# Kernel optimization log

Hardware: AMD Instinct MI355X
Metric: run time of the kernel (lower is better)

## Reference

```python
import jax, jax.numpy as jnp
import numpy as np

N_HEAD = 32
HEAD_DIM = 128
D = N_HEAD * HEAD_DIM  # 4096
B = 8
NUM_PAGES = 32
PAGE = 128


def setup_inputs() -> dict:
    key = jax.random.key(0)
    ks = jax.random.split(key, 7)
    s = 0.02
    return {
        "x": jax.random.normal(ks[0], (B, 1, D), jnp.float32),
        "k_cache": jax.random.normal(ks[1], (NUM_PAGES, B, N_HEAD, PAGE, HEAD_DIM), jnp.float32),
        "v_cache": jax.random.normal(ks[2], (NUM_PAGES, B, N_HEAD, PAGE, HEAD_DIM), jnp.float32),
        "w_attn": jax.random.normal(ks[3], (D, 3 * D), jnp.float32) * s,
        "b_attn": jax.random.normal(ks[4], (3 * D,), jnp.float32) * s,
        "w_proj": jax.random.normal(ks[5], (D, D), jnp.float32) * s,
        "b_proj": jax.random.normal(ks[6], (D,), jnp.float32) * s,
    }


def _online_attention(q, k_cache, v_cache, k_cur, v_cur):
    # q, k_cur, v_cur: [B, H, 1, hd]; caches: [P, B, H, page, hd]
    scale = 1.0 / np.sqrt(HEAD_DIM)

    def page_step(carry, kv):
        denom, y = carry  # denom: [B,H,1,1], y: [B,H,1,hd]
        k_i, v_i = kv
        S = jnp.einsum("bhqd,bhkd->bhqk", q, k_i) * scale
        P = jnp.exp(S)  # no running-max, exactly as source
        d = P.sum(axis=-1, keepdims=True)
        y = (jnp.einsum("bhqk,bhkd->bhqd", P, v_i) + denom * y) / (denom + d)
        return (denom + d, y), None

    denom0 = jnp.zeros((q.shape[0], N_HEAD, 1, 1), q.dtype)
    y0 = jnp.zeros_like(q)
    (denom, y), _ = jax.lax.scan(page_step, (denom0, y0), (k_cache, v_cache))
    # final step with current-token k, v
    S_n = jnp.einsum("bhqd,bhkd->bhqk", q, k_cur) * scale
    P_n = jnp.exp(S_n)
    d_n = P_n.sum(axis=-1, keepdims=True)
    y = (jnp.einsum("bhqk,bhkd->bhqd", P_n, v_cur) + denom * y) / (denom + d_n)
    return y


def reference(x, k_cache, v_cache, w_attn, b_attn, w_proj, b_proj):
    Bq, T, _ = x.shape  # T == 1 (decode)
    qkv = x @ w_attn + b_attn  # [B, 1, 3D]
    q, k, v = jnp.split(qkv, 3, axis=-1)
    def heads(t):
        return t.reshape(Bq, T, N_HEAD, HEAD_DIM).transpose(0, 2, 1, 3)  # [B,H,1,hd]
    q, k, v = heads(q), heads(k), heads(v)
    y = _online_attention(q, k_cache, v_cache, k, v)  # [B,H,1,hd]
    y = y.transpose(0, 2, 1, 3).reshape(Bq, 1, D)
    return y @ w_proj + b_proj
```

## Files before the change

### kernel.cpp

```cpp
#include <hip/hip_runtime.h>
#include <math.h>

#define DMODEL 4096
#define THREED 12288
#define NHEAD 32
#define HDIM 128
#define NB 8
#define NPAGES 32
#define PAGEK 128

#if __has_builtin(__builtin_amdgcn_exp2f)
#define FAST_EXP2(x) __builtin_amdgcn_exp2f(x)
#else
#define FAST_EXP2(x) exp2f(x)
#endif

#define SCALE_LOG2E (0.08838834764831845f * 1.44269504088896340736f)

__global__ __launch_bounds__(256) void gemm_skinny_partial(
    const float* __restrict__ X, const float* __restrict__ W,
    float* __restrict__ part, int K, int N, int kchunk) {
  const int col = (blockIdx.x * 256 + threadIdx.x) * 2;
  const int k0 = blockIdx.y * kchunk;

  float2 acc[8];
  #pragma unroll
  for (int b = 0; b < 8; ++b) acc[b] = make_float2(0.f, 0.f);

  const float* wp = W + (size_t)k0 * N + col;
  const float* xp = X + k0;

  #pragma unroll 8
  for (int k = 0; k < kchunk; ++k) {
    const float2 w = *(const float2*)(wp + (size_t)k * N);
    #pragma unroll
    for (int b = 0; b < 8; ++b) {
      const float xv = xp[b * K + k];
      acc[b].x += xv * w.x;
      acc[b].y += xv * w.y;
    }
  }
  #pragma unroll
  for (int b = 0; b < 8; ++b)
    *(float2*)(part + ((size_t)blockIdx.y * 8 + b) * N + col) = acc[b];
}

__global__ __launch_bounds__(256) void gemm_skinny_reduce(
    const float* __restrict__ part, const float* __restrict__ bias,
    float* __restrict__ out, int N, int ksplit) {
  int idx = blockIdx.x * 256 + threadIdx.x;
  int n4 = N >> 2;
  int b = idx / n4, col = (idx - b * n4) * 4;
  float4 acc = *(const float4*)(bias + col);
  for (int s = 0; s < ksplit; ++s) {
    const float4 p = *(const float4*)(part + ((size_t)s * 8 + b) * N + col);
    acc.x += p.x;
    acc.y += p.y;
    acc.z += p.z;
    acc.w += p.w;
  }
  *(float4*)(out + (size_t)b * N + col) = acc;
}

__global__ __launch_bounds__(256) void attn_partial(
    const float* __restrict__ qkv,
    const float* __restrict__ k_cache,
    const float* __restrict__ v_cache,
    float* __restrict__ part_y,
    float* __restrict__ part_den) {
  const int page = blockIdx.x;
  const int h = blockIdx.y;
  const int b = blockIdx.z;
  const int tid = threadIdx.x;
  const int wave = tid >> 6;
  const int lane = tid & 63;
  const int half = lane >> 5;
  const int l31 = lane & 31;

  const float4 qf =
      *(const float4*)(qkv + (size_t)b * THREED + h * HDIM + 4 * l31);

  const size_t base = ((((size_t)page * NB + b) * NHEAD + h) * PAGEK) * HDIM;
  const float* kp = k_cache + base;
  const float* vp = v_cache + base;

  float4 yacc = {0.f, 0.f, 0.f, 0.f};
  float den = 0.f;

  #pragma unroll 8
  for (int i = 0; i < 16; ++i) {
    const int key = wave * 32 + i * 2 + half;
    const float4 kf = *(const float4*)(kp + key * HDIM + 4 * l31);
    const float4 vf = *(const float4*)(vp + key * HDIM + 4 * l31);
    float s = qf.x * kf.x + qf.y * kf.y + qf.z * kf.z + qf.w * kf.w;
    s += __shfl_xor(s, 1, 64);
    s += __shfl_xor(s, 2, 64);
    s += __shfl_xor(s, 4, 64);
    s += __shfl_xor(s, 8, 64);
    s += __shfl_xor(s, 16, 64);
    const float w = FAST_EXP2(s * SCALE_LOG2E);
    den += w;
    yacc.x += w * vf.x;
    yacc.y += w * vf.y;
    yacc.z += w * vf.z;
    yacc.w += w * vf.w;
  }

  __shared__ float y_lds[8][HDIM];
  __shared__ float d_lds[8];
  const int row = wave * 2 + half;
  *(float4*)&y_lds[row][4 * l31] = yacc;
  if (l31 == 0) d_lds[row] = den;
  __syncthreads();

  if (tid < HDIM) {
    float y = 0.f;
    #pragma unroll
    for (int r = 0; r < 8; ++r) y += y_lds[r][tid];
    const int bhp = (b * NHEAD + h) * NPAGES + page;
    part_y[(size_t)bhp * HDIM + tid] = y;
    if (tid == 0) {
      float dd = 0.f;
      #pragma unroll
      for (int r = 0; r < 8; ++r) dd += d_lds[r];
      part_den[bhp] = dd;
    }
  }
}

__global__ __launch_bounds__(128) void attn_reduce(
    const float* __restrict__ qkv,
    const float* __restrict__ part_y, const float* __restrict__ part_den,
    float* __restrict__ yattn) {
  const int h = blockIdx.x;
  const int b = blockIdx.y;
  const int d = threadIdx.x;
  const int bh = b * NHEAD + h;

  float y = 0.f;
  #pragma unroll 4
  for (int p = 0; p < NPAGES; ++p)
    y += part_y[((size_t)bh * NPAGES + p) * HDIM + d];
  float den = 0.f;
  #pragma unroll 4
  for (int p = 0; p < NPAGES; ++p) den += part_den[bh * NPAGES + p];

  const float q = qkv[(size_t)b * THREED + h * HDIM + d];
  const float kc = qkv[(size_t)b * THREED + DMODEL + h * HDIM + d];
  const float vc = qkv[(size_t)b * THREED + 2 * DMODEL + h * HDIM + d];

  __shared__ float red[HDIM];
  red[d] = q * kc;
  __syncthreads();
  for (int s = 64; s > 0; s >>= 1) {
    if (d < s) red[d] += red[d + s];
    __syncthreads();
  }
  const float wn = FAST_EXP2(red[0] * SCALE_LOG2E);
  y = (y + wn * vc) / (den + wn);
  yattn[(size_t)b * DMODEL + h * HDIM + d] = y;
}

extern "C" void kernel_launch(void* const* d_in, const int* in_sizes, int n_in,
                              void* d_out, int out_size, void* d_ws,
                              size_t ws_size, hipStream_t stream) {
  const float* x = (const float*)d_in[0];
  const float* k_cache = (const float*)d_in[1];
  const float* v_cache = (const float*)d_in[2];
  const float* w_attn = (const float*)d_in[3];
  const float* b_attn = (const float*)d_in[4];
  const float* w_proj = (const float*)d_in[5];
  const float* b_proj = (const float*)d_in[6];
  float* out = (float*)d_out;
  float* ws = (float*)d_ws;

  float* qkv = ws;
  float* g1p = qkv + 98304;
  float* apy = g1p + 32 * 8 * THREED;
  float* apd = apy + 8192 * HDIM;
  float* yat = apd + 8192;
  float* g2p = yat + NB * DMODEL;

  gemm_skinny_partial<<<dim3(THREED / 512, 32), 256, 0, stream>>>(
      x, w_attn, g1p, DMODEL, THREED, 128);
  gemm_skinny_reduce<<<dim3(NB * THREED / 1024), 256, 0, stream>>>(
      g1p, b_attn, qkv, THREED, 32);

  attn_partial<<<dim3(NPAGES, NHEAD, NB), 256, 0, stream>>>(
      qkv, k_cache, v_cache, apy, apd);
  attn_reduce<<<dim3(NHEAD, NB), 128, 0, stream>>>(qkv, apy, apd, yat);

  gemm_skinny_partial<<<dim3(DMODEL / 512, 64), 256, 0, stream>>>(
      yat, w_proj, g2p, DMODEL, DMODEL, 64);
  gemm_skinny_reduce<<<dim3(NB * DMODEL / 1024), 256, 0, stream>>>(
      g2p, b_proj, out, DMODEL, 64);
}
```

Before: 275.6 us.

## Fuse QKV reduce and page-split attention into one per-head kernel

Replaces the page-split attention kernel, its reduction kernel and the QKV split-K reduce with one kernel per (head, batch). Each block first sums the split-K partials plus bias for its q/k/v slice, then loops over all pages itself. This drops two launches and the partial-result round trips through memory. In exchange, the attention grid shrinks from thousands of blocks to 256, which risks too little memory-level parallelism to stream the KV cache at full bandwidth.

```diff
diff --git a/kernel.cpp b/kernel.cpp
--- a/kernel.cpp
+++ b/kernel.cpp
@@ -62,103 +62,95 @@
   *(float4*)(out + (size_t)b * N + col) = acc;
 }
 
-__global__ __launch_bounds__(256) void attn_partial(
-    const float* __restrict__ qkv,
+__global__ __launch_bounds__(512) void attn_mono(
+    const float* __restrict__ g1p,
+    const float* __restrict__ b_attn,
     const float* __restrict__ k_cache,
     const float* __restrict__ v_cache,
-    float* __restrict__ part_y,
-    float* __restrict__ part_den) {
-  const int page = blockIdx.x;
-  const int h = blockIdx.y;
-  const int b = blockIdx.z;
+    float* __restrict__ yat) {
+  const int h = blockIdx.x;
+  const int b = blockIdx.y;
   const int tid = threadIdx.x;
-  const int wave = tid >> 6;
+
+  __shared__ float q_lds[HDIM], kc_lds[HDIM], vc_lds[HDIM];
+  __shared__ float y16[16][HDIM];
+  __shared__ float den16[16];
+  __shared__ float wn_lds;
+
+  if (tid < 384) {
+    const int which = tid >> 7;
+    const int d = tid & 127;
+    const int col = which * DMODEL + h * HDIM + d;
+    float val = b_attn[col];
+    #pragma unroll 8
+    for (int s = 0; s < 32; ++s)
+      val += g1p[((size_t)s * 8 + b) * THREED + col];
+    if (which == 0) q_lds[d] = val;
+    else if (which == 1) kc_lds[d] = val;
+    else vc_lds[d] = val;
+  }
+  __syncthreads();
+
+  if (tid < 64) {
+    float s0 = q_lds[tid] * kc_lds[tid] + q_lds[tid + 64] * kc_lds[tid + 64];
+    s0 += __shfl_xor(s0, 1, 64);
+    s0 += __shfl_xor(s0, 2, 64);
+    s0 += __shfl_xor(s0, 4, 64);
+    s0 += __shfl_xor(s0, 8, 64);
+    s0 += __shfl_xor(s0, 16, 64);
+    s0 += __shfl_xor(s0, 32, 64);
+    if (tid == 0) wn_lds = FAST_EXP2(s0 * SCALE_LOG2E);
+  }
+
+  const int wv = tid >> 6;
   const int lane = tid & 63;
   const int half = lane >> 5;
   const int l31 = lane & 31;
-
-  const float4 qf =
-      *(const float4*)(qkv + (size_t)b * THREED + h * HDIM + 4 * l31);
-
-  const size_t base = ((((size_t)page * NB + b) * NHEAD + h) * PAGEK) * HDIM;
-  const float* kp = k_cache + base;
-  const float* vp = v_cache + base;
+  const float4 qf = *(const float4*)&q_lds[4 * l31];
 
   float4 yacc = {0.f, 0.f, 0.f, 0.f};
   float den = 0.f;
 
-  #pragma unroll 8
-  for (int i = 0; i < 16; ++i) {
-    const int key = wave * 32 + i * 2 + half;
-    const float4 kf = *(const float4*)(kp + key * HDIM + 4 * l31);
-    const float4 vf = *(const float4*)(vp + key * HDIM + 4 * l31);
-    float s = qf.x * kf.x + qf.y * kf.y + qf.z * kf.z + qf.w * kf.w;
-    s += __shfl_xor(s, 1, 64);
-    s += __shfl_xor(s, 2, 64);
-    s += __shfl_xor(s, 4, 64);
-    s += __shfl_xor(s, 8, 64);
-    s += __shfl_xor(s, 16, 64);
-    const float w = FAST_EXP2(s * SCALE_LOG2E);
-    den += w;
-    yacc.x += w * vf.x;
-    yacc.y += w * vf.y;
-    yacc.z += w * vf.z;
-    yacc.w += w * vf.w;
+  for (int p = 0; p < NPAGES; ++p) {
+    const size_t base = ((((size_t)p * NB + b) * NHEAD + h) * PAGEK) * HDIM;
+    const float* kp = k_cache + base;
+    const float* vp = v_cache + base;
+    #pragma unroll 8
+    for (int i = 0; i < 8; ++i) {
+      const int key = wv * 16 + i * 2 + half;
+      const float4 kf = *(const float4*)(kp + key * HDIM + 4 * l31);
+      const float4 vf = *(const float4*)(vp + key * HDIM + 4 * l31);
+      float s = qf.x * kf.x + qf.y * kf.y + qf.z * kf.z + qf.w * kf.w;
+      s += __shfl_xor(s, 1, 64);
+      s += __shfl_xor(s, 2, 64);
+      s += __shfl_xor(s, 4, 64);
+      s += __shfl_xor(s, 8, 64);
+      s += __shfl_xor(s, 16, 64);
+      const float w = FAST_EXP2(s * SCALE_LOG2E);
+      den += w;
+      yacc.x += w * vf.x;
+      yacc.y += w * vf.y;
+      yacc.z += w * vf.z;
+      yacc.w += w * vf.w;
+    }
   }
 
-  __shared__ float y_lds[8][HDIM];
-  __shared__ float d_lds[8];
-  const int row = wave * 2 + half;
-  *(float4*)&y_lds[row][4 * l31] = yacc;
-  if (l31 == 0) d_lds[row] = den;
+  const int row = wv * 2 + half;
+  *(float4*)&y16[row][4 * l31] = yacc;
+  if (l31 == 0) den16[row] = den;
   __syncthreads();
 
   if (tid < HDIM) {
     float y = 0.f;
     #pragma unroll
-    for (int r = 0; r < 8; ++r) y += y_lds[r][tid];
-    const int bhp = (b * NHEAD + h) * NPAGES + page;
-    part_y[(size_t)bhp * HDIM + tid] = y;
-    if (tid == 0) {
-      float dd = 0.f;
-      #pragma unroll
-      for (int r = 0; r < 8; ++r) dd += d_lds[r];
-      part_den[bhp] = dd;
-    }
+    for (int r = 0; r < 16; ++r) y += y16[r][tid];
+    float dt = 0.f;
+    #pragma unroll
+    for (int r = 0; r < 16; ++r) dt += den16[r];
+    const float wn = wn_lds;
+    yat[(size_t)b * DMODEL + h * HDIM + tid] =
+        (y + wn * vc_lds[tid]) / (dt + wn);
   }
-}
-
-__global__ __launch_bounds__(128) void attn_reduce(
-    const float* __restrict__ qkv,
-    const float* __restrict__ part_y, const float* __restrict__ part_den,
-    float* __restrict__ yattn) {
-  const int h = blockIdx.x;
-  const int b = blockIdx.y;
-  const int d = threadIdx.x;
-  const int bh = b * NHEAD + h;
-
-  float y = 0.f;
-  #pragma unroll 4
-  for (int p = 0; p < NPAGES; ++p)
-    y += part_y[((size_t)bh * NPAGES + p) * HDIM + d];
-  float den = 0.f;
-  #pragma unroll 4
-  for (int p = 0; p < NPAGES; ++p) den += part_den[bh * NPAGES + p];
-
-  const float q = qkv[(size_t)b * THREED + h * HDIM + d];
-  const float kc = qkv[(size_t)b * THREED + DMODEL + h * HDIM + d];
-  const float vc = qkv[(size_t)b * THREED + 2 * DMODEL + h * HDIM + d];
-
-  __shared__ float red[HDIM];
-  red[d] = q * kc;
-  __syncthreads();
-  for (int s = 64; s > 0; s >>= 1) {
-    if (d < s) red[d] += red[d + s];
-    __syncthreads();
-  }
-  const float wn = FAST_EXP2(red[0] * SCALE_LOG2E);
-  y = (y + wn * vc) / (den + wn);
-  yattn[(size_t)b * DMODEL + h * HDIM + d] = y;
 }
 
 extern "C" void kernel_launch(void* const* d_in, const int* in_sizes, int n_in,
@@ -174,21 +166,15 @@
   float* out = (float*)d_out;
   float* ws = (float*)d_ws;
 
-  float* qkv = ws;
-  float* g1p = qkv + 98304;
-  float* apy = g1p + 32 * 8 * THREED;
-  float* apd = apy + 8192 * HDIM;
-  float* yat = apd + 8192;
+  float* g1p = ws;
+  float* yat = g1p + 32 * 8 * THREED;
   float* g2p = yat + NB * DMODEL;
 
   gemm_skinny_partial<<<dim3(THREED / 512, 32), 256, 0, stream>>>(
       x, w_attn, g1p, DMODEL, THREED, 128);
-  gemm_skinny_reduce<<<dim3(NB * THREED / 1024), 256, 0, stream>>>(
-      g1p, b_attn, qkv, THREED, 32);
 
-  attn_partial<<<dim3(NPAGES, NHEAD, NB), 256, 0, stream>>>(
-      qkv, k_cache, v_cache, apy, apd);
-  attn_reduce<<<dim3(NHEAD, NB), 128, 0, stream>>>(qkv, apy, apd, yat);
+  attn_mono<<<dim3(NHEAD, NB), 512, 0, stream>>>(
+      g1p, b_attn, k_cache, v_cache, yat);
 
   gemm_skinny_partial<<<dim3(DMODEL / 512, 64), 256, 0, stream>>>(
       yat, w_proj, g2p, DMODEL, DMODEL, 64);
```

Measured after the change: 311.5 us. 13.0% more time.

## Fuse QKV split-K reduction into attention kernels, dropping separate reduce launch

Applied to the files above, without the earlier changes.

Removes the gemm_skinny_reduce launch for the QKV projection. Each attention block now sums the split-K partials plus bias itself: q into shared memory in attn_partial, and q/k/v in attn_reduce. This saves a launch and a write/read of the qkv buffer, but every one of the many attention blocks repeats the q reduction, adding redundant L2 traffic and a sync before the KV loop. The KV loop unroll factor is also reduced.

```diff
diff --git a/kernel.cpp b/kernel.cpp
--- a/kernel.cpp
+++ b/kernel.cpp
@@ -8,6 +8,7 @@
 #define NB 8
 #define NPAGES 32
 #define PAGEK 128
+#define KSPLIT1 32
 
 #if __has_builtin(__builtin_amdgcn_exp2f)
 #define FAST_EXP2(x) __builtin_amdgcn_exp2f(x)
@@ -63,7 +64,8 @@
 }
 
 __global__ __launch_bounds__(256) void attn_partial(
-    const float* __restrict__ qkv,
+    const float* __restrict__ g1p,
+    const float* __restrict__ b_attn,
     const float* __restrict__ k_cache,
     const float* __restrict__ v_cache,
     float* __restrict__ part_y,
@@ -77,8 +79,19 @@
   const int half = lane >> 5;
   const int l31 = lane & 31;
 
-  const float4 qf =
-      *(const float4*)(qkv + (size_t)b * THREED + h * HDIM + 4 * l31);
+  __shared__ float q_lds[HDIM];
+
+  if (tid < HDIM) {
+    const int col = h * HDIM + tid;
+    float val = b_attn[col];
+    #pragma unroll
+    for (int s = 0; s < KSPLIT1; ++s)
+      val += g1p[((size_t)s * 8 + b) * THREED + col];
+    q_lds[tid] = val;
+  }
+  __syncthreads();
+
+  const float4 qf = *(const float4*)&q_lds[4 * l31];
 
   const size_t base = ((((size_t)page * NB + b) * NHEAD + h) * PAGEK) * HDIM;
   const float* kp = k_cache + base;
@@ -87,7 +100,7 @@
   float4 yacc = {0.f, 0.f, 0.f, 0.f};
   float den = 0.f;
 
-  #pragma unroll 8
+  #pragma unroll 4
   for (int i = 0; i < 16; ++i) {
     const int key = wave * 32 + i * 2 + half;
     const float4 kf = *(const float4*)(kp + key * HDIM + 4 * l31);
@@ -129,13 +142,26 @@
 }
 
 __global__ __launch_bounds__(128) void attn_reduce(
-    const float* __restrict__ qkv,
+    const float* __restrict__ g1p,
+    const float* __restrict__ b_attn,
     const float* __restrict__ part_y, const float* __restrict__ part_den,
     float* __restrict__ yattn) {
   const int h = blockIdx.x;
   const int b = blockIdx.y;
   const int d = threadIdx.x;
   const int bh = b * NHEAD + h;
+
+  const int col = h * HDIM + d;
+  float qv = b_attn[col];
+  float kc = b_attn[DMODEL + col];
+  float vc = b_attn[2 * DMODEL + col];
+  #pragma unroll 8
+  for (int s = 0; s < KSPLIT1; ++s) {
+    const size_t base = ((size_t)s * 8 + b) * THREED + col;
+    qv += g1p[base];
+    kc += g1p[base + DMODEL];
+    vc += g1p[base + 2 * DMODEL];
+  }
 
   float y = 0.f;
   #pragma unroll 4
@@ -145,12 +171,8 @@
   #pragma unroll 4
   for (int p = 0; p < NPAGES; ++p) den += part_den[bh * NPAGES + p];
 
-  const float q = qkv[(size_t)b * THREED + h * HDIM + d];
-  const float kc = qkv[(size_t)b * THREED + DMODEL + h * HDIM + d];
-  const float vc = qkv[(size_t)b * THREED + 2 * DMODEL + h * HDIM + d];
-
   __shared__ float red[HDIM];
-  red[d] = q * kc;
+  red[d] = qv * kc;
   __syncthreads();
   for (int s = 64; s > 0; s >>= 1) {
     if (d < s) red[d] += red[d + s];
@@ -174,21 +196,19 @@
   float* out = (float*)d_out;
   float* ws = (float*)d_ws;
 
-  float* qkv = ws;
-  float* g1p = qkv + 98304;
+  float* g1p = ws;
   float* apy = g1p + 32 * 8 * THREED;
   float* apd = apy + 8192 * HDIM;
   float* yat = apd + 8192;
   float* g2p = yat + NB * DMODEL;
 
-  gemm_skinny_partial<<<dim3(THREED / 512, 32), 256, 0, stream>>>(
+  gemm_skinny_partial<<<dim3(THREED / 512, KSPLIT1), 256, 0, stream>>>(
       x, w_attn, g1p, DMODEL, THREED, 128);
-  gemm_skinny_reduce<<<dim3(NB * THREED / 1024), 256, 0, stream>>>(
-      g1p, b_attn, qkv, THREED, 32);
 
   attn_partial<<<dim3(NPAGES, NHEAD, NB), 256, 0, stream>>>(
-      qkv, k_cache, v_cache, apy, apd);
-  attn_reduce<<<dim3(NHEAD, NB), 128, 0, stream>>>(qkv, apy, apd, yat);
+      g1p, b_attn, k_cache, v_cache, apy, apd);
+  attn_reduce<<<dim3(NHEAD, NB), 128, 0, stream>>>(
+      g1p, b_attn, apy, apd, yat);
 
   gemm_skinny_partial<<<dim3(DMODEL / 512, 64), 256, 0, stream>>>(
       yat, w_proj, g2p, DMODEL, DMODEL, 64);
```

New measurement: 273.0 us. No clear change (-1.0%).
